# Optimization experiments

Hardware: AMD Instinct MI355X
Metric: run time of the kernel (lower is better)

Reference implementation:

```python
import jax, jax.numpy as jnp
import numpy as np

B, S, D, F, E, K = 4, 2048, 1024, 4096, 8, 2


def setup_inputs() -> dict:
    key = jax.random.key(0)
    ks = jax.random.split(key, 8)
    x = jax.random.normal(ks[0], (B, S, D), dtype=jnp.float32)
    # torch nn.Linear stores W as (out, in); stack per-expert params on leading E axis
    router_w = jax.random.normal(ks[1], (E, D), dtype=jnp.float32) * 0.02
    w1_w = jax.random.normal(ks[2], (E, F, D), dtype=jnp.float32) * 0.02
    w1_b = jax.random.normal(ks[3], (E, F), dtype=jnp.float32) * 0.02
    w2_w = jax.random.normal(ks[4], (E, D, F), dtype=jnp.float32) * 0.02
    w2_b = jax.random.normal(ks[5], (E, D), dtype=jnp.float32) * 0.02
    wg_w = jax.random.normal(ks[6], (E, F, D), dtype=jnp.float32) * 0.02
    wg_b = jax.random.normal(ks[7], (E, F), dtype=jnp.float32) * 0.02
    return {"x": x, "router_w": router_w, "w1_w": w1_w, "w1_b": w1_b,
            "w2_w": w2_w, "w2_b": w2_b, "wg_w": wg_w, "wg_b": wg_b}


def reference(x, router_w, w1_w, w1_b, w2_w, w2_b, wg_w, wg_b):
    # router: softmax then top-k (identical to torch.topk(softmax(...)))
    probs = jax.nn.softmax(jnp.einsum('bsd,ed->bse', x, router_w), axis=-1)
    token_probs, probs_idx = jax.lax.top_k(probs, K)  # (b,s,k)
    # combine the k gate weights into a dense (b,s,E) gate (top-k indices are distinct,
    # so summing one-hot slots reproduces the original scatter + sum over k exactly)
    gates = jnp.sum(token_probs[..., None] *
                    jax.nn.one_hot(probs_idx, E, dtype=x.dtype), axis=-2)  # (b,s,E)
    gates_e = jnp.moveaxis(gates, -1, 0)  # (E,b,s)

    def body(acc, params):
        w1w, w1b, w2w, w2b, wgw, wgb, g = params
        y = jax.nn.gelu(jnp.einsum('bsd,fd->bsf', x, wgw) + wgb, approximate=False)
        h = y * (jnp.einsum('bsd,fd->bsf', x, w1w) + w1b)
        out = jnp.einsum('bsf,df->bsd', h, w2w) + w2b
        return acc + out * g[..., None], None

    acc0 = jnp.zeros_like(x)
    out, _ = jax.lax.scan(body, acc0, (w1_w, w1_b, w2_w, w2_b, wg_w, wg_b, gates_e))
    return out
```

## Files before the change

kernel.cpp:

```cpp
#include <hip/hip_runtime.h>
#include <hip/hip_bf16.h>

#define TOK 8192
#define DD 1024
#define FF 4096
#define EE 8
#define NPAIR 16384

typedef __attribute__((ext_vector_type(8))) short short8;
typedef __attribute__((ext_vector_type(4))) short short4v;
typedef __attribute__((ext_vector_type(4))) float f32x4;

#define VMCNT8()  asm volatile("s_waitcnt vmcnt(8)" ::: "memory")
#define VMCNT0()  asm volatile("s_waitcnt vmcnt(0)" ::: "memory")
#define LGKM0()   asm volatile("s_waitcnt lgkmcnt(0)" ::: "memory")
#define BARRIER() asm volatile("s_barrier" ::: "memory")
#define SCHEDB()  __builtin_amdgcn_sched_barrier(0)

__device__ __forceinline__ void async16(const void* g, void* l) {
  __builtin_amdgcn_global_load_lds((const __attribute__((address_space(1))) void*)g,
                                   (__attribute__((address_space(3))) void*)l, 16, 0, 0);
}

__device__ __forceinline__ short bfc(float f) {
  return __builtin_bit_cast(short, (__bf16)f);
}
__device__ __forceinline__ short8 cvt8(f32x4 a, f32x4 b) {
  short8 r;
  r[0]=bfc(a[0]); r[1]=bfc(a[1]); r[2]=bfc(a[2]); r[3]=bfc(a[3]);
  r[4]=bfc(b[0]); r[5]=bfc(b[1]); r[6]=bfc(b[2]); r[7]=bfc(b[3]);
  return r;
}

__global__ __launch_bounds__(256) void cvt_bf16_kernel(const float* __restrict__ src,
                                                       short* __restrict__ dst, int n8) {
  int i = blockIdx.x * 256 + threadIdx.x;
  const int stride = gridDim.x * 256;
  for (; i < n8; i += stride) {
    f32x4 a = ((const f32x4*)src)[2*i];
    f32x4 b = ((const f32x4*)src)[2*i + 1];
    ((short8*)dst)[i] = cvt8(a, b);
  }
}

__global__ __launch_bounds__(256) void cvt_interleave(const float* __restrict__ wgw,
    const float* __restrict__ w1w, short* __restrict__ wB) {
  const int b = blockIdx.x;
  const int e = b >> 12;
  const int f = b & 4095;
  const int g = f >> 4, j = f & 15;
  const int tid = threadIdx.x;
  const int u = tid & 127;
  const float* src = ((tid < 128) ? wgw : w1w) + (size_t)b * DD;
  const size_t drow = (size_t)e * (2*FF) + 32*g + j + ((tid < 128) ? 0 : 16);
  f32x4 a = ((const f32x4*)src)[2*u];
  f32x4 c = ((const f32x4*)src)[2*u + 1];
  ((short8*)(wB + drow * DD))[u] = cvt8(a, c);
}

__global__ __launch_bounds__(64) void router_kernel(const float* __restrict__ x,
    const float* __restrict__ rw, int* __restrict__ counts, int* __restrict__ lists,
    float* __restrict__ gates, int* __restrict__ eids, short* __restrict__ xb, int write_xb) {
  const int t = blockIdx.x;
  const int l = threadIdx.x;
  const f32x4* xr = (const f32x4*)(x + (size_t)t * DD);
  f32x4 xv[4];
#pragma unroll
  for (int i = 0; i < 4; i++) xv[i] = xr[l + 64 * i];
  if (write_xb) {
    short4v* xo = (short4v*)(xb + (size_t)t * DD);
#pragma unroll
    for (int i = 0; i < 4; i++) {
      short4v o; o[0]=bfc(xv[i][0]); o[1]=bfc(xv[i][1]); o[2]=bfc(xv[i][2]); o[3]=bfc(xv[i][3]);
      xo[l + 64 * i] = o;
    }
  }
  float lg[EE];
#pragma unroll
  for (int e = 0; e < EE; e++) {
    const f32x4* wr = (const f32x4*)(rw + e * DD);
    float s = 0.f;
#pragma unroll
    for (int i = 0; i < 4; i++) {
      f32x4 w = wr[l + 64 * i];
      s += xv[i][0]*w[0] + xv[i][1]*w[1] + xv[i][2]*w[2] + xv[i][3]*w[3];
    }
#pragma unroll
    for (int off = 32; off > 0; off >>= 1) s += __shfl_down(s, off, 64);
    lg[e] = s;
  }
  if (l == 0) {
    float mx = lg[0];
#pragma unroll
    for (int e = 1; e < EE; e++) mx = fmaxf(mx, lg[e]);
    float p[EE]; float den = 0.f;
#pragma unroll
    for (int e = 0; e < EE; e++) { p[e] = expf(lg[e] - mx); den += p[e]; }
    int i1 = 0;
#pragma unroll
    for (int e = 1; e < EE; e++) if (p[e] > p[i1]) i1 = e;
    int i2 = (i1 == 0) ? 1 : 0;
#pragma unroll
    for (int e = 0; e < EE; e++) if (e != i1 && p[e] > p[i2]) i2 = e;
    float inv = 1.f / den;
    gates[t*2+0] = p[i1] * inv;  eids[t*2+0] = i1;
    gates[t*2+1] = p[i2] * inv;  eids[t*2+1] = i2;
    int p1 = atomicAdd(&counts[i1], 1); lists[i1*TOK + p1] = t*2 + 0;
    int p2 = atomicAdd(&counts[i2], 1); lists[i2*TOK + p2] = t*2 + 1;
  }
}

#define TB2 32768

#define STG2(buf, t) do { const int ko=(t)*64;                                 \
    _Pragma("unroll")                                                          \
    for (int p = 0; p < 4; p++) {                                              \
      async16(aS[p] + ko, &ldsm[(buf)*TB2 + p*4096 + wid*512]);                \
      async16(bS[p] + ko, &ldsm[(buf)*TB2 + 16384 + p*4096 + wid*512]);        \
    } } while(0)

#define RD_A(buf, kk, mi) (*(const short8*)&ldsm[(buf)*TB2 + (wr*128+(mi)*16+ln15)*64 + ((((kk)*4+g) ^ ((wr*128+(mi)*16+ln15)&7))*8)])
#define RD_B(buf, kk, ni) (*(const short8*)&ldsm[(buf)*TB2 + 16384 + (wc*64+(ni)*16+ln15)*64 + ((((kk)*4+g) ^ ((wc*64+(ni)*16+ln15)&7))*8)])

#define MFMA_BF16 __builtin_amdgcn_mfma_f32_16x16x32_bf16

#define KLOOP3(NT)                                                             \
  STG2(0, 0);                                                                  \
  SCHEDB();                                                                    \
  _Pragma("unroll 1")                                                          \
  for (int t = 0; t < (NT); t++) {                                             \
    const int cur = t & 1;                                                     \
    if (t + 1 < (NT)) {                                                        \
      STG2(cur ^ 1, t + 1);                                                    \
      SCHEDB();                                                                \
      VMCNT8();                                                                \
    } else {                                                                   \
      VMCNT0();                                                                \
    }                                                                          \
    SCHEDB();                                                                  \
    __builtin_amdgcn_s_barrier();                                              \
    SCHEDB();                                                                  \
    _Pragma("unroll")                                                          \
    for (int kk = 0; kk < 2; kk++) {                                           \
      short8 a[8], b[4];                                                       \
      _Pragma("unroll")                                                        \
      for (int mi = 0; mi < 8; mi++) a[mi] = RD_A(cur, kk, mi);                \
      _Pragma("unroll")                                                        \
      for (int ni = 0; ni < 4; ni++) b[ni] = RD_B(cur, kk, ni);                \
      __builtin_amdgcn_s_setprio(1);                                           \
      _Pragma("unroll")                                                        \
      for (int mi = 0; mi < 8; mi++)                                           \
        _Pragma("unroll")                                                      \
        for (int ni = 0; ni < 4; ni++)                                         \
          acc[mi][ni] = MFMA_BF16(a[mi], b[ni], acc[mi][ni], 0, 0, 0);         \
      __builtin_amdgcn_s_setprio(0);                                           \
    }                                                                          \
    SCHEDB();                                                                  \
    LGKM0();                                                                   \
    SCHEDB();                                                                  \
    __builtin_amdgcn_s_barrier();                                              \
    SCHEDB();                                                                  \
  }                                                                            \
  VMCNT0();

__global__ __launch_bounds__(512, 1) void stage_a8(
    const short* __restrict__ xb, const short* __restrict__ wB,
    const float* __restrict__ wgb, const float* __restrict__ w1b,
    const int* __restrict__ counts, const int* __restrict__ lists,
    short* __restrict__ hbuf, int f0chunk, int Fc) {

  const int NBX = gridDim.x, NBY = gridDim.y;
  const int q = NBX * NBY;
  const int lin = blockIdx.x + NBX * (blockIdx.y + NBY * blockIdx.z);
  const int orig = (lin & 7) * q + (lin >> 3);
  const int e = orig / q;
  const int m = orig - e * q;
  const int by = m % NBY;
  const int bx = m / NBY;

  const int cnt = counts[e];
  const int row0 = bx * 256;
  if (row0 >= cnt) return;
  const int R0 = f0chunk * 2 + by * 256;

  __shared__ short ldsm[2 * TB2];
  __shared__ int s_pair[256];

  const int tid = threadIdx.x;
  const int wid = tid >> 6;
  const int lane = tid & 63;
  const int ln15 = lane & 15, g = lane >> 4;
  const int wr = wid >> 2, wc = wid & 3;

  if (tid < 256) {
    int r = row0 + tid;
    s_pair[tid] = (r < cnt) ? lists[e*TOK + r] : 0;
  }
  __syncthreads();

  const short* aS[4]; const short* bS[4];
#pragma unroll
  for (int p = 0; p < 4; p++) {
    int j = p * 512 + tid;
    int r = j >> 3;
    int sl = (j & 7) ^ (r & 7);
    aS[p] = xb + (size_t)(s_pair[r] >> 1) * DD + sl * 8;
    bS[p] = wB + ((size_t)e * (2*FF) + R0 + r) * DD + sl * 8;
  }

  f32x4 acc[8][4] = {};

  KLOOP3(16)

  const float* wgb_e = wgb + e * FF;
  const float* w1b_e = w1b + e * FF;
  float bgv[2], b1v[2]; int fl[2];
#pragma unroll
  for (int m2 = 0; m2 < 2; m2++) {
    int fg = (R0 + wc*64 + m2*32) / 2 + ln15;
    bgv[m2] = wgb_e[fg];
    b1v[m2] = w1b_e[fg];
    fl[m2] = fg - f0chunk;
  }
#pragma unroll
  for (int mi = 0; mi < 8; mi++) {
    int trb = wr*128 + mi*16 + (g << 2);
#pragma unroll
    for (int m2 = 0; m2 < 2; m2++) {
#pragma unroll
      for (int j = 0; j < 4; j++) {
        int tr = trb + j;
        if (row0 + tr < cnt) {
          int pair = s_pair[tr];
          float hg = acc[mi][2*m2][j] + bgv[m2];
          float h1 = acc[mi][2*m2+1][j] + b1v[m2];
          float gl = 0.5f * hg * (1.f + erff(hg * 0.70710678118f));
          hbuf[(size_t)pair * Fc + fl[m2]] = bfc(gl * h1);
        }
      }
    }
  }
}

__global__ __launch_bounds__(512, 1) void stage_b8(
    const short* __restrict__ hbuf, const short* __restrict__ w2wb,
    const int* __restrict__ counts, const int* __restrict__ lists,
    float* __restrict__ ybuf, int Fc) {

  const int NBX = gridDim.x, NBY = gridDim.y;
  const int q = NBX * NBY;
  const int lin = blockIdx.x + NBX * (blockIdx.y + NBY * blockIdx.z);
  const int orig = (lin & 7) * q + (lin >> 3);
  const int e = orig / q;
  const int m = orig - e * q;
  const int by = m % NBY;
  const int bx = m / NBY;

  const int cnt = counts[e];
  const int row0 = bx * 256;
  if (row0 >= cnt) return;
  const int d0 = by * 256;

  __shared__ short ldsm[2 * TB2];
  __shared__ int s_pair[256];

  const int tid = threadIdx.x;
  const int wid = tid >> 6;
  const int lane = tid & 63;
  const int ln15 = lane & 15, g = lane >> 4;
  const int wr = wid >> 2, wc = wid & 3;

  if (tid < 256) {
    int r = row0 + tid;
    s_pair[tid] = (r < cnt) ? lists[e*TOK + r] : 0;
  }
  __syncthreads();

  const short* aS[4]; const short* bS[4];
#pragma unroll
  for (int p = 0; p < 4; p++) {
    int j = p * 512 + tid;
    int r = j >> 3;
    int sl = (j & 7) ^ (r & 7);
    aS[p] = hbuf + (size_t)s_pair[r] * Fc + sl * 8;
    bS[p] = w2wb + ((size_t)e * DD + d0 + r) * FF + sl * 8;
  }

  f32x4 acc[8][4] = {};
  const int NT = Fc >> 6;

  KLOOP3(NT)

#pragma unroll
  for (int mi = 0; mi < 8; mi++) {
    int trb = wr*128 + mi*16 + (g << 2);
#pragma unroll
    for (int j = 0; j < 4; j++) {
      int tr = trb + j;
      if (row0 + tr < cnt) {
        int pair = s_pair[tr];
        float* yrow = ybuf + (size_t)pair * DD;
#pragma unroll
        for (int ni = 0; ni < 4; ni++) {
          int d = d0 + wc*64 + ni*16 + ln15;
          yrow[d] = acc[mi][ni][j];
        }
      }
    }
  }
}

__global__ __launch_bounds__(256) void combine_kernel(const float* __restrict__ yb,
    const float* __restrict__ w2b, const float* __restrict__ gates,
    const int* __restrict__ eids, float* __restrict__ out) {
  const int t = blockIdx.x;
  const int tid = threadIdx.x;
  const float g0 = gates[2*t], g1 = gates[2*t+1];
  const int e0 = eids[2*t], e1 = eids[2*t+1];
  f32x4 y0 = ((const f32x4*)(yb + (size_t)(2*t) * DD))[tid];
  f32x4 y1 = ((const f32x4*)(yb + (size_t)(2*t+1) * DD))[tid];
  f32x4 c0 = ((const f32x4*)(w2b + (size_t)e0 * DD))[tid];
  f32x4 c1 = ((const f32x4*)(w2b + (size_t)e1 * DD))[tid];
  f32x4 o;
#pragma unroll
  for (int i = 0; i < 4; i++) o[i] = g0 * (y0[i] + c0[i]) + g1 * (y1[i] + c1[i]);
  ((f32x4*)(out + (size_t)t * DD))[tid] = o;
}

#define BB_LDS (128*64)
__global__ __launch_bounds__(256, 2) void stage_b_bf(
    const short* __restrict__ hbuf, const short* __restrict__ w2wb, const float* __restrict__ w2b,
    const int* __restrict__ counts, const int* __restrict__ lists, const float* __restrict__ gates,
    float* __restrict__ out, int f0chunk, int Fc, int addbias) {

  const int lin = blockIdx.x + 64 * (blockIdx.y + 8 * blockIdx.z);
  const int orig = (lin & 7) * 512 + (lin >> 3);
  const int bx = orig & 63;
  const int by = (orig >> 6) & 7;
  const int e  = orig >> 9;

  const int cnt = counts[e];
  const int row0 = bx * 128;
  if (row0 >= cnt) return;
  const int d0 = by * 128;

  __shared__ short lA[2 * BB_LDS];
  __shared__ short lB[2 * BB_LDS];
  __shared__ int s_pair[128];

  const int tid = threadIdx.x;
  const int wid = tid >> 6;
  const int lane = tid & 63;

  if (tid < 128) {
    int r = row0 + tid;
    s_pair[tid] = (r < cnt) ? lists[e*TOK + r] : 0;
  }
  __syncthreads();

  const short* aSrc[4]; const short* bSrc[4];
#pragma unroll
  for (int p = 0; p < 4; p++) {
    int j = p * 256 + tid;
    int r = j >> 3;
    int sl = (j & 7) ^ (r & 7);
    aSrc[p] = hbuf + (size_t)s_pair[r] * Fc + sl * 8;
    bSrc[p] = w2wb + ((size_t)e * DD + d0 + r) * FF + f0chunk + sl * 8;
  }

  f32x4 acc[4][4] = {};
  const int wr = wid >> 1, wc = wid & 1;
  const int NT = Fc >> 6;

#pragma unroll
  for (int p = 0; p < 4; p++) async16(aSrc[p], &lA[p*2048 + wid*512]);
#pragma unroll
  for (int p = 0; p < 4; p++) async16(bSrc[p], &lB[p*2048 + wid*512]);

  for (int t = 0; t < NT; t++) {
    const int cur = t & 1;
    if (t + 1 < NT) {
      const int nb = cur ^ 1;
      const int kf = (t + 1) * 64;
#pragma unroll
      for (int p = 0; p < 4; p++) async16(aSrc[p] + kf, &lA[nb*BB_LDS + p*2048 + wid*512]);
#pragma unroll
      for (int p = 0; p < 4; p++) async16(bSrc[p] + kf, &lB[nb*BB_LDS + p*2048 + wid*512]);
      VMCNT8();
    } else {
      VMCNT0();
    }
    BARRIER();

    const short* LA = lA + cur * BB_LDS;
    const short* LB = lB + cur * BB_LDS;
#pragma unroll
    for (int kk = 0; kk < 2; kk++) {
      short8 a[4], b[4];
#pragma unroll
      for (int mi = 0; mi < 4; mi++) {
        int r = wr*64 + mi*16 + (lane & 15);
        int u = (kk*4 + (lane >> 4)) ^ (r & 7);
        a[mi] = *(const short8*)(LA + r*64 + u*8);
      }
#pragma unroll
      for (int ni = 0; ni < 4; ni++) {
        int r = wc*64 + ni*16 + (lane & 15);
        int u = (kk*4 + (lane >> 4)) ^ (r & 7);
        b[ni] = *(const short8*)(LB + r*64 + u*8);
      }
#pragma unroll
      for (int mi = 0; mi < 4; mi++)
#pragma unroll
        for (int ni = 0; ni < 4; ni++)
          acc[mi][ni] = MFMA_BF16(a[mi], b[ni], acc[mi][ni], 0, 0, 0);
    }
    BARRIER();
  }

  const float* w2b_e = w2b + e * DD;
#pragma unroll
  for (int mi = 0; mi < 4; mi++) {
    int trb = wr*64 + mi*16 + ((lane >> 4) << 2);
#pragma unroll
    for (int j = 0; j < 4; j++) {
      int tr = trb + j;
      if (row0 + tr < cnt) {
        int pair = s_pair[tr];
        int t = pair >> 1;
        float gt = gates[pair];
        float* orow = out + (size_t)t * DD;
#pragma unroll
        for (int ni = 0; ni < 4; ni++) {
          int d = d0 + wc*64 + ni*16 + (lane & 15);
          float v = acc[mi][ni][j] * gt;
          if (addbias) v += w2b_e[d] * gt;
          atomicAdd(orow + d, v);
        }
      }
    }
  }
}

__global__ __launch_bounds__(256, 2) void stage_a_f32(
    const float* __restrict__ x, const float* __restrict__ wgw, const float* __restrict__ wgb,
    const float* __restrict__ w1w, const float* __restrict__ w1b,
    const int* __restrict__ counts, const int* __restrict__ lists,
    short* __restrict__ hbuf, int f0chunk, int Fc) {

  const int e = blockIdx.z;
  const int cnt = counts[e];
  const int row0 = blockIdx.x * 128;
  if (row0 >= cnt) return;
  const int fc0 = blockIdx.y * 128;
  const int fg0 = f0chunk + fc0;

  __shared__ float lA[128 * 32];
  __shared__ float lBg[128 * 32];
  __shared__ float lB1[128 * 32];
  __shared__ int s_pair[128];

  const int tid = threadIdx.x;
  const int wid = tid >> 6;
  const int lane = tid & 63;

  if (tid < 128) {
    int r = row0 + tid;
    s_pair[tid] = (r < cnt) ? lists[e*TOK + r] : 0;
  }
  __syncthreads();

  const float* aSrc[4]; const float* gSrc[4]; const float* oSrc[4];
#pragma unroll
  for (int p = 0; p < 4; p++) {
    int j = p * 256 + tid;
    int r = j >> 3;
    int sl = (j & 7) ^ (r & 7);
    aSrc[p] = x + (size_t)(s_pair[r] >> 1) * DD + sl * 4;
    gSrc[p] = wgw + ((size_t)e * FF + fg0 + r) * DD + sl * 4;
    oSrc[p] = w1w + ((size_t)e * FF + fg0 + r) * DD + sl * 4;
  }

  f32x4 accg[4][4] = {}; f32x4 acc1[4][4] = {};
  const int wr = wid >> 1, wc = wid & 1;

  for (int k0 = 0; k0 < DD; k0 += 32) {
#pragma unroll
    for (int p = 0; p < 4; p++) async16(aSrc[p] + k0, &lA[p*1024 + wid*256]);
#pragma unroll
    for (int p = 0; p < 4; p++) async16(gSrc[p] + k0, &lBg[p*1024 + wid*256]);
#pragma unroll
    for (int p = 0; p < 4; p++) async16(oSrc[p] + k0, &lB1[p*1024 + wid*256]);
    __syncthreads();

    short8 a[4], bg[4], b1[4];
#pragma unroll
    for (int mi = 0; mi < 4; mi++) {
      int r = wr*64 + mi*16 + (lane & 15);
      int g2 = (lane >> 4) * 2;
      const f32x4* Ar = (const f32x4*)&lA[r * 32];
      a[mi] = cvt8(Ar[g2 ^ (r & 7)], Ar[(g2 + 1) ^ (r & 7)]);
    }
#pragma unroll
    for (int ni = 0; ni < 4; ni++) {
      int r = wc*64 + ni*16 + (lane & 15);
      int g2 = (lane >> 4) * 2;
      const f32x4* Bg = (const f32x4*)&lBg[r * 32];
      const f32x4* B1 = (const f32x4*)&lB1[r * 32];
      bg[ni] = cvt8(Bg[g2 ^ (r & 7)], Bg[(g2 + 1) ^ (r & 7)]);
      b1[ni] = cvt8(B1[g2 ^ (r & 7)], B1[(g2 + 1) ^ (r & 7)]);
    }
#pragma unroll
    for (int mi = 0; mi < 4; mi++)
#pragma unroll
      for (int ni = 0; ni < 4; ni++) {
        accg[mi][ni] = MFMA_BF16(a[mi], bg[ni], accg[mi][ni], 0, 0, 0);
        acc1[mi][ni] = MFMA_BF16(a[mi], b1[ni], acc1[mi][ni], 0, 0, 0);
      }
    __syncthreads();
  }

  const float* wgb_e = wgb + e * FF;
  const float* w1b_e = w1b + e * FF;
#pragma unroll
  for (int mi = 0; mi < 4; mi++) {
    int trb = wr*64 + mi*16 + ((lane >> 4) << 2);
#pragma unroll
    for (int ni = 0; ni < 4; ni++) {
      int c = wc*64 + ni*16 + (lane & 15);
      float bgv = wgb_e[fg0 + c];
      float b1v = w1b_e[fg0 + c];
#pragma unroll
      for (int j = 0; j < 4; j++) {
        int tr = trb + j;
        if (row0 + tr < cnt) {
          int pair = s_pair[tr];
          float hg = accg[mi][ni][j] + bgv;
          float h1 = acc1[mi][ni][j] + b1v;
          float gl = 0.5f * hg * (1.f + erff(hg * 0.70710678118f));
          hbuf[(size_t)pair * Fc + fc0 + c] = bfc(gl * h1);
        }
      }
    }
  }
}

__global__ __launch_bounds__(256, 2) void stage_b_f32(
    const short* __restrict__ hbuf, const float* __restrict__ w2w, const float* __restrict__ w2b,
    const int* __restrict__ counts, const int* __restrict__ lists, const float* __restrict__ gates,
    float* __restrict__ out, int f0chunk, int Fc, int addbias) {

  const int e = blockIdx.z;
  const int cnt = counts[e];
  const int row0 = blockIdx.x * 128;
  if (row0 >= cnt) return;
  const int d0 = blockIdx.y * 128;

  __shared__ short lA[128 * 64];
  __shared__ float lB[128 * 64];
  __shared__ int s_pair[128];

  const int tid = threadIdx.x;
  const int wid = tid >> 6;
  const int lane = tid & 63;

  if (tid < 128) {
    int r = row0 + tid;
    s_pair[tid] = (r < cnt) ? lists[e*TOK + r] : 0;
  }
  __syncthreads();

  const short* aSrc[4];
#pragma unroll
  for (int p = 0; p < 4; p++) {
    int j = p * 256 + tid;
    int r = j >> 3;
    int sl = (j & 7) ^ (r & 7);
    aSrc[p] = hbuf + (size_t)s_pair[r] * Fc + sl * 8;
  }
  const float* bSrc[8];
#pragma unroll
  for (int p = 0; p < 8; p++) {
    int j = p * 256 + tid;
    int r = j >> 4;
    int sl = (j & 15) ^ (r & 7);
    bSrc[p] = w2w + ((size_t)e * DD + d0 + r) * FF + f0chunk + sl * 4;
  }

  f32x4 acc[4][4] = {};
  const int wr = wid >> 1, wc = wid & 1;

  for (int kf = 0; kf < Fc; kf += 64) {
#pragma unroll
    for (int p = 0; p < 4; p++) async16(aSrc[p] + kf, &lA[p*2048 + wid*512]);
#pragma unroll
    for (int p = 0; p < 8; p++) async16(bSrc[p] + kf, &lB[p*1024 + wid*256]);
    __syncthreads();

#pragma unroll
    for (int kk = 0; kk < 2; kk++) {
      short8 a[4]; short8 b[4];
#pragma unroll
      for (int mi = 0; mi < 4; mi++) {
        int r = wr*64 + mi*16 + (lane & 15);
        int u = (kk*4 + (lane >> 4)) ^ (r & 7);
        a[mi] = ((const short8*)(lA + r * 64))[u];
      }
#pragma unroll
      for (int ni = 0; ni < 4; ni++) {
        int r = wc*64 + ni*16 + (lane & 15);
        int g2 = (kk*4 + (lane >> 4)) * 2;
        const f32x4* Br = (const f32x4*)(lB + r * 64);
        b[ni] = cvt8(Br[g2 ^ (r & 7)], Br[(g2 + 1) ^ (r & 7)]);
      }
#pragma unroll
      for (int mi = 0; mi < 4; mi++)
#pragma unroll
        for (int ni = 0; ni < 4; ni++)
          acc[mi][ni] = MFMA_BF16(a[mi], b[ni], acc[mi][ni], 0, 0, 0);
    }
    __syncthreads();
  }

  const float* w2b_e = w2b + e * DD;
#pragma unroll
  for (int mi = 0; mi < 4; mi++) {
    int trb = wr*64 + mi*16 + ((lane >> 4) << 2);
#pragma unroll
    for (int j = 0; j < 4; j++) {
      int tr = trb + j;
      if (row0 + tr < cnt) {
        int pair = s_pair[tr];
        int t = pair >> 1;
        float gt = gates[pair];
        float* orow = out + (size_t)t * DD;
#pragma unroll
        for (int ni = 0; ni < 4; ni++) {
          int d = d0 + wc*64 + ni*16 + (lane & 15);
          float v = acc[mi][ni][j] * gt;
          if (addbias) v += w2b_e[d] * gt;
          atomicAdd(orow + d, v);
        }
      }
    }
  }
}

extern "C" void kernel_launch(void* const* d_in, const int* in_sizes, int n_in,
                              void* d_out, int out_size, void* d_ws, size_t ws_size,
                              hipStream_t stream) {
  const float* x   = (const float*)d_in[0];
  const float* rw  = (const float*)d_in[1];
  const float* w1w = (const float*)d_in[2];
  const float* w1b = (const float*)d_in[3];
  const float* w2w = (const float*)d_in[4];
  const float* w2b = (const float*)d_in[5];
  const float* wgw = (const float*)d_in[6];
  const float* wgb = (const float*)d_in[7];
  float* out = (float*)d_out;

  char* ws = (char*)d_ws;
  size_t off = 0;
  int* counts = (int*)(ws + off); off += 128;
  int* lists  = (int*)(ws + off); off += (size_t)EE * TOK * 4;
  float* gates = (float*)(ws + off); off += (size_t)NPAIR * 4;
  int* eids = (int*)(ws + off); off += (size_t)NPAIR * 4;
  const size_t base0 = off;

  const size_t WELEM = (size_t)EE * FF * DD;
  const size_t bf_need = base0 + (size_t)TOK*DD*2 + 2*WELEM*2 + WELEM*2;

  hipMemsetAsync(counts, 0, 128, stream);

  const int cands[6] = {4096, 2048, 1024, 512, 256, 128};

  if (bf_need + (size_t)NPAIR * 128 * 2 <= ws_size) {
    off = base0;
    short* xb   = (short*)(ws + off); off += (size_t)TOK * DD * 2;
    short* wB   = (short*)(ws + off); off += 2 * WELEM * 2;
    short* w2wb = (short*)(ws + off); off += WELEM * 2;
    short* hbuf = (short*)(ws + off);
    float* ybuf = (float*)wB;

    int Fc = 128;
    for (int i = 0; i < 6; i++)
      if (off + (size_t)NPAIR * cands[i] * 2 <= ws_size) { Fc = cands[i]; break; }

    router_kernel<<<dim3(TOK), dim3(64), 0, stream>>>(x, rw, counts, lists, gates, eids, xb, 1);
    cvt_interleave<<<dim3(EE*FF), dim3(256), 0, stream>>>(wgw, w1w, wB);
    cvt_bf16_kernel<<<dim3(2048), dim3(256), 0, stream>>>(w2w, w2wb, (int)(WELEM/8));

    if (Fc == 4096) {
      stage_a8<<<dim3(32, (2*Fc)/256, EE), dim3(512), 0, stream>>>(
          xb, wB, wgb, w1b, counts, lists, hbuf, 0, Fc);
      stage_b8<<<dim3(32, DD/256, EE), dim3(512), 0, stream>>>(
          hbuf, w2wb, counts, lists, ybuf, Fc);
      combine_kernel<<<dim3(TOK), dim3(256), 0, stream>>>(ybuf, w2b, gates, eids, out);
    } else {
      hipMemsetAsync(out, 0, (size_t)TOK * DD * 4, stream);
      for (int f0 = 0; f0 < FF; f0 += Fc) {
        stage_a8<<<dim3(32, (2*Fc)/256, EE), dim3(512), 0, stream>>>(
            xb, wB, wgb, w1b, counts, lists, hbuf, f0, Fc);
        stage_b_bf<<<dim3(64, DD/128, EE), dim3(256), 0, stream>>>(
            hbuf, w2wb, w2b, counts, lists, gates, out, f0, Fc, f0 == 0);
      }
    }
  } else {
    short* hbuf = (short*)(ws + base0);
    int Fc = 128;
    for (int i = 0; i < 6; i++)
      if (base0 + (size_t)NPAIR * cands[i] * 2 <= ws_size) { Fc = cands[i]; break; }

    hipMemsetAsync(out, 0, (size_t)TOK * DD * 4, stream);
    router_kernel<<<dim3(TOK), dim3(64), 0, stream>>>(x, rw, counts, lists, gates, eids, nullptr, 0);

    for (int f0 = 0; f0 < FF; f0 += Fc) {
      dim3 ga(64, Fc / 128, EE);
      stage_a_f32<<<ga, dim3(256), 0, stream>>>(x, wgw, wgb, w1w, w1b, counts, lists, hbuf, f0, Fc);
      dim3 gb(64, DD / 128, EE);
      stage_b_f32<<<gb, dim3(256), 0, stream>>>(hbuf, w2w, w2b, counts, lists, gates, out, f0, Fc, f0 == 0);
    }
  }
}
```

Before: 1.053 ms.

## Replace 256x256 double-buffered MFMA GEMMs with 128x128 single-buffered tiles at higher occupancy

Both expert GEMM stages move from 512-thread blocks with 256x256 output tiles and a double-buffered LDS pipeline to 256-thread blocks with 128x128 tiles. Each k-step now does a load, sync, compute, sync in a single LDS buffer, and the launch bounds allow three blocks per CU. Latency hiding shifts from explicit prefetch to having more resident blocks. Nontemporal loads and stores are also added to the conversion, output and combine kernels. The smaller tiles reduce data reuse per block and add global/LDS traffic, and the explicit overlap of loads with MFMA work is lost.

```diff
diff --git a/kernel.cpp b/kernel.cpp
--- a/kernel.cpp
+++ b/kernel.cpp
@@ -13,9 +13,7 @@
 
 #define VMCNT8()  asm volatile("s_waitcnt vmcnt(8)" ::: "memory")
 #define VMCNT0()  asm volatile("s_waitcnt vmcnt(0)" ::: "memory")
-#define LGKM0()   asm volatile("s_waitcnt lgkmcnt(0)" ::: "memory")
 #define BARRIER() asm volatile("s_barrier" ::: "memory")
-#define SCHEDB()  __builtin_amdgcn_sched_barrier(0)
 
 __device__ __forceinline__ void async16(const void* g, void* l) {
   __builtin_amdgcn_global_load_lds((const __attribute__((address_space(1))) void*)g,
@@ -32,13 +30,15 @@
   return r;
 }
 
+#define MFMA_BF16 __builtin_amdgcn_mfma_f32_16x16x32_bf16
+
 __global__ __launch_bounds__(256) void cvt_bf16_kernel(const float* __restrict__ src,
                                                        short* __restrict__ dst, int n8) {
   int i = blockIdx.x * 256 + threadIdx.x;
   const int stride = gridDim.x * 256;
   for (; i < n8; i += stride) {
-    f32x4 a = ((const f32x4*)src)[2*i];
-    f32x4 b = ((const f32x4*)src)[2*i + 1];
+    f32x4 a = __builtin_nontemporal_load(&((const f32x4*)src)[2*i]);
+    f32x4 b = __builtin_nontemporal_load(&((const f32x4*)src)[2*i + 1]);
     ((short8*)dst)[i] = cvt8(a, b);
   }
 }
@@ -53,8 +53,8 @@
   const int u = tid & 127;
   const float* src = ((tid < 128) ? wgw : w1w) + (size_t)b * DD;
   const size_t drow = (size_t)e * (2*FF) + 32*g + j + ((tid < 128) ? 0 : 16);
-  f32x4 a = ((const f32x4*)src)[2*u];
-  f32x4 c = ((const f32x4*)src)[2*u + 1];
+  f32x4 a = __builtin_nontemporal_load(&((const f32x4*)src)[2*u]);
+  f32x4 c = __builtin_nontemporal_load(&((const f32x4*)src)[2*u + 1]);
   ((short8*)(wB + drow * DD))[u] = cvt8(a, c);
 }
 
@@ -110,60 +110,8 @@
   }
 }
 
-#define TB2 32768
-
-#define STG2(buf, t) do { const int ko=(t)*64;                                 \
-    _Pragma("unroll")                                                          \
-    for (int p = 0; p < 4; p++) {                                              \
-      async16(aS[p] + ko, &ldsm[(buf)*TB2 + p*4096 + wid*512]);                \
-      async16(bS[p] + ko, &ldsm[(buf)*TB2 + 16384 + p*4096 + wid*512]);        \
-    } } while(0)
-
-#define RD_A(buf, kk, mi) (*(const short8*)&ldsm[(buf)*TB2 + (wr*128+(mi)*16+ln15)*64 + ((((kk)*4+g) ^ ((wr*128+(mi)*16+ln15)&7))*8)])
-#define RD_B(buf, kk, ni) (*(const short8*)&ldsm[(buf)*TB2 + 16384 + (wc*64+(ni)*16+ln15)*64 + ((((kk)*4+g) ^ ((wc*64+(ni)*16+ln15)&7))*8)])
-
-#define MFMA_BF16 __builtin_amdgcn_mfma_f32_16x16x32_bf16
-
-#define KLOOP3(NT)                                                             \
-  STG2(0, 0);                                                                  \
-  SCHEDB();                                                                    \
-  _Pragma("unroll 1")                                                          \
-  for (int t = 0; t < (NT); t++) {                                             \
-    const int cur = t & 1;                                                     \
-    if (t + 1 < (NT)) {                                                        \
-      STG2(cur ^ 1, t + 1);                                                    \
-      SCHEDB();                                                                \
-      VMCNT8();                                                                \
-    } else {                                                                   \
-      VMCNT0();                                                                \
-    }                                                                          \
-    SCHEDB();                                                                  \
-    __builtin_amdgcn_s_barrier();                                              \
-    SCHEDB();                                                                  \
-    _Pragma("unroll")                                                          \
-    for (int kk = 0; kk < 2; kk++) {                                           \
-      short8 a[8], b[4];                                                       \
-      _Pragma("unroll")                                                        \
-      for (int mi = 0; mi < 8; mi++) a[mi] = RD_A(cur, kk, mi);                \
-      _Pragma("unroll")                                                        \
-      for (int ni = 0; ni < 4; ni++) b[ni] = RD_B(cur, kk, ni);                \
-      __builtin_amdgcn_s_setprio(1);                                           \
-      _Pragma("unroll")                                                        \
-      for (int mi = 0; mi < 8; mi++)                                           \
-        _Pragma("unroll")                                                      \
-        for (int ni = 0; ni < 4; ni++)                                         \
-          acc[mi][ni] = MFMA_BF16(a[mi], b[ni], acc[mi][ni], 0, 0, 0);         \
-      __builtin_amdgcn_s_setprio(0);                                           \
-    }                                                                          \
-    SCHEDB();                                                                  \
-    LGKM0();                                                                   \
-    SCHEDB();                                                                  \
-    __builtin_amdgcn_s_barrier();                                              \
-    SCHEDB();                                                                  \
-  }                                                                            \
-  VMCNT0();
-
-__global__ __launch_bounds__(512, 1) void stage_a8(
+
+__global__ __launch_bounds__(256, 3) void stage_a97(
     const short* __restrict__ xb, const short* __restrict__ wB,
     const float* __restrict__ wgb, const float* __restrict__ w1b,
     const int* __restrict__ counts, const int* __restrict__ lists,
@@ -179,20 +127,21 @@
   const int bx = m / NBY;
 
   const int cnt = counts[e];
-  const int row0 = bx * 256;
+  const int row0 = bx * 128;
   if (row0 >= cnt) return;
-  const int R0 = f0chunk * 2 + by * 256;
-
-  __shared__ short ldsm[2 * TB2];
-  __shared__ int s_pair[256];
+  const int R0 = f0chunk * 2 + by * 128;
+
+  __shared__ short lA[128 * 64];
+  __shared__ short lB[128 * 64];
+  __shared__ int s_pair[128];
 
   const int tid = threadIdx.x;
   const int wid = tid >> 6;
   const int lane = tid & 63;
   const int ln15 = lane & 15, g = lane >> 4;
-  const int wr = wid >> 2, wc = wid & 3;
-
-  if (tid < 256) {
+  const int wr = wid >> 1, wc = wid & 1;
+
+  if (tid < 128) {
     int r = row0 + tid;
     s_pair[tid] = (r < cnt) ? lists[e*TOK + r] : 0;
   }
@@ -201,16 +150,44 @@
   const short* aS[4]; const short* bS[4];
 #pragma unroll
   for (int p = 0; p < 4; p++) {
-    int j = p * 512 + tid;
+    int j = p * 256 + tid;
     int r = j >> 3;
     int sl = (j & 7) ^ (r & 7);
     aS[p] = xb + (size_t)(s_pair[r] >> 1) * DD + sl * 8;
     bS[p] = wB + ((size_t)e * (2*FF) + R0 + r) * DD + sl * 8;
   }
 
-  f32x4 acc[8][4] = {};
-
-  KLOOP3(16)
+  f32x4 acc[4][4] = {};
+
+  for (int t = 0; t < 16; t++) {
+    const int ko = t * 64;
+#pragma unroll
+    for (int p = 0; p < 4; p++) {
+      async16(aS[p] + ko, &lA[p*2048 + wid*512]);
+      async16(bS[p] + ko, &lB[p*2048 + wid*512]);
+    }
+    __syncthreads();
+#pragma unroll
+    for (int kk = 0; kk < 2; kk++) {
+      short8 a[4], b[4];
+#pragma unroll
+      for (int mi = 0; mi < 4; mi++) {
+        int r = wr*64 + mi*16 + ln15;
+        a[mi] = *(const short8*)&lA[r*64 + (((kk*4 + g) ^ (r & 7)) * 8)];
+      }
+#pragma unroll
+      for (int ni = 0; ni < 4; ni++) {
+        int r = wc*64 + ni*16 + ln15;
+        b[ni] = *(const short8*)&lB[r*64 + (((kk*4 + g) ^ (r & 7)) * 8)];
+      }
+#pragma unroll
+      for (int mi = 0; mi < 4; mi++)
+#pragma unroll
+        for (int ni = 0; ni < 4; ni++)
+          acc[mi][ni] = MFMA_BF16(a[mi], b[ni], acc[mi][ni], 0, 0, 0);
+    }
+    __syncthreads();
+  }
 
   const float* wgb_e = wgb + e * FF;
   const float* w1b_e = w1b + e * FF;
@@ -223,8 +200,8 @@
     fl[m2] = fg - f0chunk;
   }
 #pragma unroll
-  for (int mi = 0; mi < 8; mi++) {
-    int trb = wr*128 + mi*16 + (g << 2);
+  for (int mi = 0; mi < 4; mi++) {
+    int trb = wr*64 + mi*16 + (g << 2);
 #pragma unroll
     for (int m2 = 0; m2 < 2; m2++) {
 #pragma unroll
@@ -235,14 +212,14 @@
           float hg = acc[mi][2*m2][j] + bgv[m2];
           float h1 = acc[mi][2*m2+1][j] + b1v[m2];
           float gl = 0.5f * hg * (1.f + erff(hg * 0.70710678118f));
-          hbuf[(size_t)pair * Fc + fl[m2]] = bfc(gl * h1);
+          __builtin_nontemporal_store(bfc(gl * h1), &hbuf[(size_t)pair * Fc + fl[m2]]);
         }
       }
     }
   }
 }
 
-__global__ __launch_bounds__(512, 1) void stage_b8(
+__global__ __launch_bounds__(256, 3) void stage_b97(
     const short* __restrict__ hbuf, const short* __restrict__ w2wb,
     const int* __restrict__ counts, const int* __restrict__ lists,
     float* __restrict__ ybuf, int Fc) {
@@ -257,20 +234,21 @@
   const int bx = m / NBY;
 
   const int cnt = counts[e];
-  const int row0 = bx * 256;
+  const int row0 = bx * 128;
   if (row0 >= cnt) return;
-  const int d0 = by * 256;
-
-  __shared__ short ldsm[2 * TB2];
-  __shared__ int s_pair[256];
+  const int d0 = by * 128;
+
+  __shared__ short lA[128 * 64];
+  __shared__ short lB[128 * 64];
+  __shared__ int s_pair[128];
 
   const int tid = threadIdx.x;
   const int wid = tid >> 6;
   const int lane = tid & 63;
   const int ln15 = lane & 15, g = lane >> 4;
-  const int wr = wid >> 2, wc = wid & 3;
-
-  if (tid < 256) {
+  const int wr = wid >> 1, wc = wid & 1;
+
+  if (tid < 128) {
     int r = row0 + tid;
     s_pair[tid] = (r < cnt) ? lists[e*TOK + r] : 0;
   }
@@ -279,21 +257,49 @@
   const short* aS[4]; const short* bS[4];
 #pragma unroll
   for (int p = 0; p < 4; p++) {
-    int j = p * 512 + tid;
+    int j = p * 256 + tid;
     int r = j >> 3;
     int sl = (j & 7) ^ (r & 7);
     aS[p] = hbuf + (size_t)s_pair[r] * Fc + sl * 8;
     bS[p] = w2wb + ((size_t)e * DD + d0 + r) * FF + sl * 8;
   }
 
-  f32x4 acc[8][4] = {};
+  f32x4 acc[4][4] = {};
   const int NT = Fc >> 6;
 
-  KLOOP3(NT)
-
-#pragma unroll
-  for (int mi = 0; mi < 8; mi++) {
-    int trb = wr*128 + mi*16 + (g << 2);
+  for (int t = 0; t < NT; t++) {
+    const int ko = t * 64;
+#pragma unroll
+    for (int p = 0; p < 4; p++) {
+      async16(aS[p] + ko, &lA[p*2048 + wid*512]);
+      async16(bS[p] + ko, &lB[p*2048 + wid*512]);
+    }
+    __syncthreads();
+#pragma unroll
+    for (int kk = 0; kk < 2; kk++) {
+      short8 a[4], b[4];
+#pragma unroll
+      for (int mi = 0; mi < 4; mi++) {
+        int r = wr*64 + mi*16 + ln15;
+        a[mi] = *(const short8*)&lA[r*64 + (((kk*4 + g) ^ (r & 7)) * 8)];
+      }
+#pragma unroll
+      for (int ni = 0; ni < 4; ni++) {
+        int r = wc*64 + ni*16 + ln15;
+        b[ni] = *(const short8*)&lB[r*64 + (((kk*4 + g) ^ (r & 7)) * 8)];
+      }
+#pragma unroll
+      for (int mi = 0; mi < 4; mi++)
+#pragma unroll
+        for (int ni = 0; ni < 4; ni++)
+          acc[mi][ni] = MFMA_BF16(a[mi], b[ni], acc[mi][ni], 0, 0, 0);
+    }
+    __syncthreads();
+  }
+
+#pragma unroll
+  for (int mi = 0; mi < 4; mi++) {
+    int trb = wr*64 + mi*16 + (g << 2);
 #pragma unroll
     for (int j = 0; j < 4; j++) {
       int tr = trb + j;
@@ -303,7 +309,7 @@
 #pragma unroll
         for (int ni = 0; ni < 4; ni++) {
           int d = d0 + wc*64 + ni*16 + ln15;
-          yrow[d] = acc[mi][ni][j];
+          __builtin_nontemporal_store(acc[mi][ni][j], &yrow[d]);
         }
       }
     }
@@ -317,14 +323,14 @@
   const int tid = threadIdx.x;
   const float g0 = gates[2*t], g1 = gates[2*t+1];
   const int e0 = eids[2*t], e1 = eids[2*t+1];
-  f32x4 y0 = ((const f32x4*)(yb + (size_t)(2*t) * DD))[tid];
-  f32x4 y1 = ((const f32x4*)(yb + (size_t)(2*t+1) * DD))[tid];
+  f32x4 y0 = __builtin_nontemporal_load(&((const f32x4*)(yb + (size_t)(2*t) * DD))[tid]);
+  f32x4 y1 = __builtin_nontemporal_load(&((const f32x4*)(yb + (size_t)(2*t+1) * DD))[tid]);
   f32x4 c0 = ((const f32x4*)(w2b + (size_t)e0 * DD))[tid];
   f32x4 c1 = ((const f32x4*)(w2b + (size_t)e1 * DD))[tid];
   f32x4 o;
 #pragma unroll
   for (int i = 0; i < 4; i++) o[i] = g0 * (y0[i] + c0[i]) + g1 * (y1[i] + c1[i]);
-  ((f32x4*)(out + (size_t)t * DD))[tid] = o;
+  __builtin_nontemporal_store(o, &((f32x4*)(out + (size_t)t * DD))[tid]);
 }
 
 #define BB_LDS (128*64)
@@ -691,15 +697,15 @@
     cvt_bf16_kernel<<<dim3(2048), dim3(256), 0, stream>>>(w2w, w2wb, (int)(WELEM/8));
 
     if (Fc == 4096) {
-      stage_a8<<<dim3(32, (2*Fc)/256, EE), dim3(512), 0, stream>>>(
+      stage_a97<<<dim3(64, (2*Fc)/128, EE), dim3(256), 0, stream>>>(
           xb, wB, wgb, w1b, counts, lists, hbuf, 0, Fc);
-      stage_b8<<<dim3(32, DD/256, EE), dim3(512), 0, stream>>>(
+      stage_b97<<<dim3(64, DD/128, EE), dim3(256), 0, stream>>>(
           hbuf, w2wb, counts, lists, ybuf, Fc);
       combine_kernel<<<dim3(TOK), dim3(256), 0, stream>>>(ybuf, w2b, gates, eids, out);
     } else {
       hipMemsetAsync(out, 0, (size_t)TOK * DD * 4, stream);
       for (int f0 = 0; f0 < FF; f0 += Fc) {
-        stage_a8<<<dim3(32, (2*Fc)/256, EE), dim3(512), 0, stream>>>(
+        stage_a97<<<dim3(64, (2*Fc)/128, EE), dim3(256), 0, stream>>>(
             xb, wB, wgb, w1b, counts, lists, hbuf, f0, Fc);
         stage_b_bf<<<dim3(64, DD/128, EE), dim3(256), 0, stream>>>(
             hbuf, w2wb, w2b, counts, lists, gates, out, f0, Fc, f0 == 0);
```

Measured after the change: 880.3 us. 1.2x faster.
